# Optimization experiments

Measured on AMD Instinct MI355X. Metric: run time of the kernel, lower is better.

Reference implementation:

```python
import jax, jax.numpy as jnp
import numpy as np

K = 7          # local window
STRIDE = 1
PAD = 3
M = 8          # channel groups
C = 256
CQ = C // M    # key/query channels (32)
MID = int(0.5 * CQ)  # geometry prior hidden (16)
B, H, W = 4, 56, 56


def _unfold(x, k, stride, pad):
    """torch.nn.Unfold equivalent -> (B, C, L, k, k) with L = ho*wo."""
    b, c, h, w = x.shape
    xp = jnp.pad(x, ((0, 0), (0, 0), (pad, pad), (pad, pad)))
    ho = (h + 2 * pad - k) // stride + 1
    wo = (w + 2 * pad - k) // stride + 1
    cols = jnp.stack(
        [xp[:, :, i:i + stride * ho:stride, j:j + stride * wo:stride]
         for i in range(k) for j in range(k)], axis=-1)  # (B,C,ho,wo,k*k)
    return cols.reshape(b, c, ho * wo, k, k), ho, wo


def _geometry_position(k):
    a = jnp.arange(-(k // 2), k // 2 + 1, dtype=jnp.float32)
    x_pos = jnp.broadcast_to(a[None, :], (k, k))
    b_r = jnp.arange(k // 2, -(k // 2) - 1, -1, dtype=jnp.float32)
    y_pos = jnp.broadcast_to(b_r[:, None], (k, k))
    return jnp.stack([x_pos, y_pos], axis=0)  # (2, k, k)


def setup_inputs() -> dict:
    key = jax.random.key(0)
    ks = jax.random.split(key, 12)
    s = 0.05
    return {
        "x": jax.random.normal(ks[0], (B, C, H, W), jnp.float32),
        "w_k": jax.random.normal(ks[1], (CQ, C), jnp.float32) * s,
        "b_k": jax.random.normal(ks[2], (CQ,), jnp.float32) * s,
        "w_q": jax.random.normal(ks[3], (CQ, C), jnp.float32) * s,
        "b_q": jax.random.normal(ks[4], (CQ,), jnp.float32) * s,
        "w_g1": jax.random.normal(ks[5], (MID, 2), jnp.float32) * s,
        "b_g1": jax.random.normal(ks[6], (MID,), jnp.float32) * s,
        "w_g2": jax.random.normal(ks[7], (CQ, MID), jnp.float32) * s,
        "b_g2": jax.random.normal(ks[8], (CQ,), jnp.float32) * s,
        "w_f": jax.random.normal(ks[9], (C, C), jnp.float32) * s,
        "b_f": jax.random.normal(ks[10], (C,), jnp.float32) * s,
    }


def reference(x, w_k, b_k, w_q, b_q, w_g1, b_g1, w_g2, b_g2, w_f, b_f):
    b = x.shape[0]
    # key/query maps: 1x1 convs C -> CQ
    km = jnp.einsum('bchw,oc->bohw', x, w_k) + b_k[None, :, None, None]
    qm = jnp.einsum('bchw,oc->bohw', x, w_q) + b_q[None, :, None, None]

    km_u, ho, wo = _unfold(km, K, STRIDE, PAD)   # (B,CQ,L,k,k)
    qm_u, _, _ = _unfold(qm, K, STRIDE, PAD)
    center = K * K // 2
    q_center = qm_u.reshape(b, CQ, ho * wo, K * K)[:, :, :, center]  # (B,CQ,L)
    ak = km_u * q_center[:, :, :, None, None]    # (B,CQ,L,k,k)

    # geometry prior: two 1x1 convs on (2,k,k) position grid
    pos = _geometry_position(K)                                   # (2,k,k)
    g1 = jax.nn.relu(jnp.einsum('pij,op->oij', pos, w_g1) + b_g1[:, None, None])
    gpk = jnp.einsum('pij,op->oij', g1, w_g2) + b_g2[:, None, None]  # (CQ,k,k)

    # NOTE: softmax over the LAST k dim only (faithful to original dim=-1)
    ck = jax.nn.softmax(ak + gpk[None, :, None, :, :], axis=-1)   # (B,CQ,L,k,k)

    x_u, _, _ = _unfold(x, K, STRIDE, PAD)                        # (B,C,L,k,k)
    x_u = x_u.reshape(b, M, CQ, ho * wo, K, K)
    # ck broadcasts across the m groups
    pre = jnp.einsum('bclij,bgclij->bgcl', ck, x_u)               # (B,M,CQ,L)
    pre = pre.reshape(b, C, ho, wo)

    out = jnp.einsum('bchw,oc->bohw', pre, w_f) + b_f[None, :, None, None]
    return out
```

## Files before the change

kernel.cpp:

```cpp
#include <hip/hip_runtime.h>
#include <hip/hip_bf16.h>

typedef __hip_bfloat16 bf16;
typedef __attribute__((ext_vector_type(8))) short short8;
typedef __attribute__((ext_vector_type(4))) float floatx4;

#define B_   4
#define C_   256
#define CQ_  32
#define MID_ 16
#define HW_  3136

__device__ __forceinline__ unsigned short f2bf(float f) {
    __hip_bfloat16 h = __float2bfloat16(f);
    return *(unsigned short*)&h;
}
__device__ __forceinline__ float bf2f(short s) {
    return __uint_as_float(((unsigned)(unsigned short)s) << 16);
}

__global__ void __launch_bounds__(256) kq_setup(const float* __restrict__ x,
        const float* __restrict__ w_k, const float* __restrict__ b_k,
        const float* __restrict__ w_q, const float* __restrict__ b_q,
        const float* __restrict__ w_f,
        const float* __restrict__ wg1, const float* __restrict__ bg1,
        const float* __restrict__ wg2, const float* __restrict__ bg2,
        float* __restrict__ km, float* __restrict__ qm,
        short* __restrict__ wfp, float* __restrict__ gpk) {
    int bid = blockIdx.x, t = threadIdx.x;
    if (bid >= 392) {
        if (bid < 408) {
            int base = (bid - 392) * 4096;
            #pragma unroll
            for (int s = 0; s < 16; s++) {
                int j = base + s * 256 + t;
                wfp[j] = (short)f2bf(w_f[(j >> 8) * 256 + (j & 7) * 32 + ((j & 255) >> 3)]);
            }
        } else {
            for (int idx = t; idx < CQ_ * 49; idx += 256) {
                int cq = idx / 49, ij = idx % 49;
                int i = ij / 7, j = ij % 7;
                float xp = (float)(j - 3), yp = (float)(3 - i);
                float acc = bg2[cq];
                #pragma unroll
                for (int o = 0; o < MID_; o++) {
                    float g1 = wg1[o * 2] * xp + wg1[o * 2 + 1] * yp + bg1[o];
                    acc += wg2[cq * MID_ + o] * fmaxf(g1, 0.f);
                }
                gpk[idx] = acc;
            }
        }
        return;
    }
    __shared__ short lt[32 * 264];
    int hw0 = (bid % 98) * 32;
    int b   = bid / 98;

    int pq = t & 7, cb = t >> 3;
    const float* xb = x + (size_t)b * C_ * HW_ + hw0 + pq * 4;
    floatx4 fa[4], fb[4];
    #pragma unroll
    for (int ii = 0; ii < 4; ii++) {
        int c = ii * 64 + cb * 2;
        fa[ii] = *(const floatx4*)(xb + (size_t)c * HW_);
        fb[ii] = *(const floatx4*)(xb + (size_t)(c + 1) * HW_);
    }
    #pragma unroll
    for (int ii = 0; ii < 4; ii++) {
        int c = ii * 64 + cb * 2;
        int c8 = c >> 3, sub = c & 7;
        #pragma unroll
        for (int u = 0; u < 4; u++) {
            int px = pq * 4 + u;
            unsigned uu = (unsigned)f2bf(fa[ii][u]) | ((unsigned)f2bf(fb[ii][u]) << 16);
            *(unsigned*)&lt[px * 264 + ((c8 + (px >> 2)) & 31) * 8 + sub] = uu;
        }
    }

    int wave = t >> 6, lane = t & 63, quad = lane >> 4, nl = lane & 15;
    int m0 = wave * 16;
    int row = m0 + nl;
    const float* wsrc = (row < 32) ? (w_k + row * C_) : (w_q + (row - 32) * C_);
    short8 af[8];
    #pragma unroll
    for (int k0 = 0; k0 < 8; k0++) {
        floatx4 wa = *(const floatx4*)(wsrc + k0 * 32 + quad * 8);
        floatx4 wb = *(const floatx4*)(wsrc + k0 * 32 + quad * 8 + 4);
        short8 v;
        #pragma unroll
        for (int u = 0; u < 4; u++) { v[u] = (short)f2bf(wa[u]); v[u + 4] = (short)f2bf(wb[u]); }
        af[k0] = v;
    }
    __syncthreads();

    floatx4 acc0 = {0.f,0.f,0.f,0.f}, acc1 = {0.f,0.f,0.f,0.f};
    #pragma unroll
    for (int nt = 0; nt < 2; nt++) {
        int px = nt * 16 + nl;
        int prow = px * 264, sw = px >> 2;
        #pragma unroll
        for (int k0 = 0; k0 < 8; k0++) {
            short8 bfr = *(const short8*)&lt[prow + (((k0 * 4 + quad) + sw) & 31) * 8];
            if (nt == 0) acc0 = __builtin_amdgcn_mfma_f32_16x16x32_bf16(af[k0], bfr, acc0, 0, 0, 0);
            else         acc1 = __builtin_amdgcn_mfma_f32_16x16x32_bf16(af[k0], bfr, acc1, 0, 0, 0);
        }
    }
    #pragma unroll
    for (int r = 0; r < 4; r++) {
        int ch = m0 + quad * 4 + r;
        bool isK = (ch < 32);
        int c = isK ? ch : ch - 32;
        float bias = isK ? b_k[c] : b_q[c];
        float* dst = (isK ? km : qm) + ((size_t)b * CQ_ + c) * HW_ + hw0 + nl;
        dst[0]  = acc0[r] + bias;
        dst[16] = acc1[r] + bias;
    }
}

__global__ void __launch_bounds__(448) core_kernel(const float* __restrict__ x,
        const float* __restrict__ km, const float* __restrict__ qm,
        const float* __restrict__ gpk, short* __restrict__ pret) {
    __shared__ float kms[14 * 64];
    __shared__ short xs[14 * 64 * 8];

    int ht = blockIdx.x, cq = blockIdx.y, b = blockIdx.z;
    int h0 = ht * 8, t = threadIdx.x;

    const float* kmc = km + ((size_t)b * CQ_ + cq) * HW_;
    if (t < 196) {
        int rr = t / 14, s = t % 14;
        int gh = h0 + rr - 3;
        floatx4 v = {0.f,0.f,0.f,0.f};
        if ((unsigned)gh < 56u) v = *(const floatx4*)&kmc[gh * 56 + s * 4];
        *(floatx4*)&kms[rr * 64 + 4 + 4 * s] = v;
    }
    if (t < 84) {
        int rr = t / 6, e = t % 6;
        kms[rr * 64 + ((e < 3) ? 1 + e : 57 + e)] = 0.f;
    }
    if (t < 392) {
        int rr = t / 28, rem = t % 28, s = rem >> 1, mg = rem & 1;
        int gh = h0 + rr - 3;
        bool valid = ((unsigned)gh < 56u);
        floatx4 f[4];
        #pragma unroll
        for (int mm = 0; mm < 4; mm++) {
            int m = mg * 4 + mm;
            f[mm] = (floatx4){0.f,0.f,0.f,0.f};
            if (valid) f[mm] = *(const floatx4*)&x[((size_t)b * C_ + m * CQ_ + cq) * HW_ + gh * 56 + s * 4];
        }
        #pragma unroll
        for (int u = 0; u < 4; u++) {
            int p = 4 + 4 * s + u;
            unsigned lo = (unsigned)f2bf(f[0][u]) | ((unsigned)f2bf(f[1][u]) << 16);
            unsigned hi = (unsigned)f2bf(f[2][u]) | ((unsigned)f2bf(f[3][u]) << 16);
            unsigned long long pk = (unsigned long long)lo | ((unsigned long long)hi << 32);
            *(unsigned long long*)&xs[(rr * 64 + p) * 8 + mg * 4] = pk;
        }
    }
    if (t < 168) {
        int rr = t / 12, rem = t % 12, e = rem >> 1, mg = rem & 1;
        int p = (e < 3) ? 1 + e : 57 + e;
        *(unsigned long long*)&xs[(rr * 64 + p) * 8 + mg * 4] = 0ull;
    }
    __syncthreads();

    int r = t / 56, w = t % 56;
    float q = qm[((size_t)b * CQ_ + cq) * HW_ + (h0 + r) * 56 + w];
    const float* gp = gpk + cq * 49;

    float acc[8];
    #pragma unroll
    for (int m = 0; m < 8; m++) acc[m] = 0.f;

    #pragma unroll
    for (int i = 0; i < 7; i++) {
        const float* kr = &kms[(r + i) * 64 + w + 1];
        float v[7], s = 0.f;
        #pragma unroll
        for (int j = 0; j < 7; j++) {
            v[j] = __expf(kr[j] * q + gp[i * 7 + j]);
            s += v[j];
        }
        float rm[8];
        #pragma unroll
        for (int m = 0; m < 8; m++) rm[m] = 0.f;
        #pragma unroll
        for (int j = 0; j < 7; j++) {
            short8 xv = *(const short8*)&xs[((r + i) * 64 + w + j + 1) * 8];
            #pragma unroll
            for (int m = 0; m < 8; m++) rm[m] += v[j] * bf2f(xv[m]);
        }
        float inv = 1.0f / s;
        #pragma unroll
        for (int m = 0; m < 8; m++) acc[m] += inv * rm[m];
    }

    short8 o8;
    #pragma unroll
    for (int m = 0; m < 8; m++) o8[m] = (short)f2bf(acc[m]);
    *(short8*)&pret[((size_t)b * HW_ + (h0 + r) * 56 + w) * C_ + cq * 8] = o8;
}

__global__ void __launch_bounds__(256) fconv_mfma(const short* __restrict__ pret,
                                                  const short* __restrict__ wfp,
                                                  const float* __restrict__ b_f,
                                                  float* __restrict__ out) {
    int hw0 = blockIdx.x * 64;
    int bm  = blockIdx.y;
    int b   = blockIdx.z;
    int t   = threadIdx.x, wave = t >> 6, lane = t & 63, quad = lane >> 4, nl = lane & 15;
    int m0  = bm * 64 + wave * 16;

    const short* arow = wfp + (m0 + nl) * C_ + quad * 8;
    short8 af[8];
    #pragma unroll
    for (int k0 = 0; k0 < 8; k0++) af[k0] = *(const short8*)(arow + k0 * 32);

    floatx4 acc[4];
    #pragma unroll
    for (int nt = 0; nt < 4; nt++) acc[nt] = (floatx4){0.f,0.f,0.f,0.f};

    const short* pb = pret + ((size_t)b * HW_ + hw0 + nl) * C_ + quad * 8;
    #pragma unroll
    for (int nt = 0; nt < 4; nt++) {
        const short* bp = pb + (size_t)nt * 16 * C_;
        #pragma unroll
        for (int k0 = 0; k0 < 8; k0++)
            acc[nt] = __builtin_amdgcn_mfma_f32_16x16x32_bf16(af[k0], *(const short8*)(bp + k0 * 32),
                                                              acc[nt], 0, 0, 0);
    }

    #pragma unroll
    for (int r = 0; r < 4; r++) {
        int ch = m0 + quad * 4 + r;
        float bias = b_f[ch];
        float* dst = out + ((size_t)b * C_ + ch) * HW_ + hw0 + nl;
        #pragma unroll
        for (int nt = 0; nt < 4; nt++)
            dst[nt * 16] = acc[nt][r] + bias;
    }
}

extern "C" void kernel_launch(void* const* d_in, const int* in_sizes, int n_in,
                              void* d_out, int out_size, void* d_ws, size_t ws_size,
                              hipStream_t stream) {
    const float* x    = (const float*)d_in[0];
    const float* w_k  = (const float*)d_in[1];
    const float* b_k  = (const float*)d_in[2];
    const float* w_q  = (const float*)d_in[3];
    const float* b_q  = (const float*)d_in[4];
    const float* w_g1 = (const float*)d_in[5];
    const float* b_g1 = (const float*)d_in[6];
    const float* w_g2 = (const float*)d_in[7];
    const float* b_g2 = (const float*)d_in[8];
    const float* w_f  = (const float*)d_in[9];
    const float* b_f  = (const float*)d_in[10];
    float* out = (float*)d_out;

    float* ws   = (float*)d_ws;
    float* km   = ws;
    float* qm   = km + (size_t)B_ * CQ_ * HW_;
    float* gpk  = qm + (size_t)B_ * CQ_ * HW_;
    short* wfp  = (short*)(gpk + CQ_ * 49);
    short* pret = wfp + C_ * C_;

    kq_setup<<<dim3(409), 256, 0, stream>>>(x, w_k, b_k, w_q, b_q, w_f,
                                            w_g1, b_g1, w_g2, b_g2, km, qm, wfp, gpk);
    core_kernel<<<dim3(7, CQ_, B_), 448, 0, stream>>>(x, km, qm, gpk, pret);
    fconv_mfma<<<dim3(HW_ / 64, C_ / 64, B_), 256, 0, stream>>>(pret, wfp, b_f, out);
}
```

Measured before the change: 148.0 us.

## Pre-transpose x to bf16 grouped layout and store km/qm as bf16

The first kernel now also writes a bf16 copy of x laid out as (b, cq, pixel, m), with the 8 group channels packed together. It also stores the key and query maps in bf16 instead of fp32, and the 1x1 conv tiles shrink to 16 pixels so more blocks run. The core kernel loads this packed data with single 16-byte reads, and each of its 256 threads (224 active) computes two output rows. This removes the strided fp32 gathers and in-kernel conversion in the core kernel, at the cost of an extra write and read of the transposed x and lower km/qm precision.

```diff
diff --git a/kernel.cpp b/kernel.cpp
--- a/kernel.cpp
+++ b/kernel.cpp
@@ -19,18 +19,34 @@
     return __uint_as_float(((unsigned)(unsigned short)s) << 16);
 }
 
-__global__ void __launch_bounds__(256) kq_setup(const float* __restrict__ x,
+__global__ void __launch_bounds__(256) k1_kernel(const float* __restrict__ x,
         const float* __restrict__ w_k, const float* __restrict__ b_k,
         const float* __restrict__ w_q, const float* __restrict__ b_q,
         const float* __restrict__ w_f,
         const float* __restrict__ wg1, const float* __restrict__ bg1,
         const float* __restrict__ wg2, const float* __restrict__ bg2,
-        float* __restrict__ km, float* __restrict__ qm,
-        short* __restrict__ wfp, float* __restrict__ gpk) {
+        short* __restrict__ km, short* __restrict__ qm,
+        short* __restrict__ xt, short* __restrict__ wfp, float* __restrict__ gpk) {
     int bid = blockIdx.x, t = threadIdx.x;
-    if (bid >= 392) {
-        if (bid < 408) {
-            int base = (bid - 392) * 4096;
+
+    if (bid >= 784) {
+        if (bid < 980) {
+            int bid2 = bid - 784;
+            int s = bid2 % 49, b = bid2 / 49;
+            int px = s * 64 + (t & 63);
+            int cg = t >> 6;
+            const float* xb = x + (size_t)b * C_ * HW_ + px;
+            #pragma unroll
+            for (int cqi = 0; cqi < 8; cqi++) {
+                int cq = cg * 8 + cqi;
+                short8 v;
+                #pragma unroll
+                for (int m = 0; m < 8; m++)
+                    v[m] = (short)f2bf(xb[(size_t)(m * CQ_ + cq) * HW_]);
+                *(short8*)&xt[(((size_t)b * CQ_ + cq) * HW_ + px) * 8] = v;
+            }
+        } else if (bid < 996) {
+            int base = (bid - 980) * 4096;
             #pragma unroll
             for (int s = 0; s < 16; s++) {
                 int j = base + s * 256 + t;
@@ -52,30 +68,17 @@
         }
         return;
     }
-    __shared__ short lt[32 * 264];
-    int hw0 = (bid % 98) * 32;
-    int b   = bid / 98;
-
-    int pq = t & 7, cb = t >> 3;
+
+    __shared__ short lt[16 * 264];
+    int hw0 = (bid % 196) * 16;
+    int b   = bid / 196;
+
+    int pq = t & 3, cb = t >> 2;
     const float* xb = x + (size_t)b * C_ * HW_ + hw0 + pq * 4;
-    floatx4 fa[4], fb[4];
-    #pragma unroll
-    for (int ii = 0; ii < 4; ii++) {
-        int c = ii * 64 + cb * 2;
-        fa[ii] = *(const floatx4*)(xb + (size_t)c * HW_);
-        fb[ii] = *(const floatx4*)(xb + (size_t)(c + 1) * HW_);
-    }
-    #pragma unroll
-    for (int ii = 0; ii < 4; ii++) {
-        int c = ii * 64 + cb * 2;
-        int c8 = c >> 3, sub = c & 7;
-        #pragma unroll
-        for (int u = 0; u < 4; u++) {
-            int px = pq * 4 + u;
-            unsigned uu = (unsigned)f2bf(fa[ii][u]) | ((unsigned)f2bf(fb[ii][u]) << 16);
-            *(unsigned*)&lt[px * 264 + ((c8 + (px >> 2)) & 31) * 8 + sub] = uu;
-        }
-    }
+    floatx4 f[4];
+    #pragma unroll
+    for (int ii = 0; ii < 4; ii++)
+        f[ii] = *(const floatx4*)(xb + (size_t)(cb * 4 + ii) * HW_);
 
     int wave = t >> 6, lane = t & 63, quad = lane >> 4, nl = lane & 15;
     int m0 = wave * 16;
@@ -91,19 +94,26 @@
         for (int u = 0; u < 4; u++) { v[u] = (short)f2bf(wa[u]); v[u + 4] = (short)f2bf(wb[u]); }
         af[k0] = v;
     }
+
+    #pragma unroll
+    for (int pr = 0; pr < 2; pr++) {
+        int c = cb * 4 + pr * 2;
+        int c8 = c >> 3, sub = c & 7;
+        #pragma unroll
+        for (int u = 0; u < 4; u++) {
+            int px = pq * 4 + u;
+            unsigned uu = (unsigned)f2bf(f[pr * 2][u]) | ((unsigned)f2bf(f[pr * 2 + 1][u]) << 16);
+            *(unsigned*)&lt[px * 264 + ((c8 + pq) & 31) * 8 + sub] = uu;
+        }
+    }
     __syncthreads();
 
-    floatx4 acc0 = {0.f,0.f,0.f,0.f}, acc1 = {0.f,0.f,0.f,0.f};
-    #pragma unroll
-    for (int nt = 0; nt < 2; nt++) {
-        int px = nt * 16 + nl;
-        int prow = px * 264, sw = px >> 2;
-        #pragma unroll
-        for (int k0 = 0; k0 < 8; k0++) {
-            short8 bfr = *(const short8*)&lt[prow + (((k0 * 4 + quad) + sw) & 31) * 8];
-            if (nt == 0) acc0 = __builtin_amdgcn_mfma_f32_16x16x32_bf16(af[k0], bfr, acc0, 0, 0, 0);
-            else         acc1 = __builtin_amdgcn_mfma_f32_16x16x32_bf16(af[k0], bfr, acc1, 0, 0, 0);
-        }
+    floatx4 acc = {0.f, 0.f, 0.f, 0.f};
+    int prow = nl * 264, sw = nl >> 2;
+    #pragma unroll
+    for (int k0 = 0; k0 < 8; k0++) {
+        short8 bfr = *(const short8*)&lt[prow + (((k0 * 4 + quad) + sw) & 31) * 8];
+        acc = __builtin_amdgcn_mfma_f32_16x16x32_bf16(af[k0], bfr, acc, 0, 0, 0);
     }
     #pragma unroll
     for (int r = 0; r < 4; r++) {
@@ -111,14 +121,13 @@
         bool isK = (ch < 32);
         int c = isK ? ch : ch - 32;
         float bias = isK ? b_k[c] : b_q[c];
-        float* dst = (isK ? km : qm) + ((size_t)b * CQ_ + c) * HW_ + hw0 + nl;
-        dst[0]  = acc0[r] + bias;
-        dst[16] = acc1[r] + bias;
-    }
-}
-
-__global__ void __launch_bounds__(448) core_kernel(const float* __restrict__ x,
-        const float* __restrict__ km, const float* __restrict__ qm,
+        short* dst = (isK ? km : qm) + ((size_t)b * CQ_ + c) * HW_ + hw0 + nl;
+        dst[0] = (short)f2bf(acc[r] + bias);
+    }
+}
+
+__global__ void __launch_bounds__(256, 4) core_kernel(const short* __restrict__ xt,
+        const short* __restrict__ km, const short* __restrict__ qm,
         const float* __restrict__ gpk, short* __restrict__ pret) {
     __shared__ float kms[14 * 64];
     __shared__ short xs[14 * 64 * 8];
@@ -126,80 +135,64 @@
     int ht = blockIdx.x, cq = blockIdx.y, b = blockIdx.z;
     int h0 = ht * 8, t = threadIdx.x;
 
-    const float* kmc = km + ((size_t)b * CQ_ + cq) * HW_;
-    if (t < 196) {
-        int rr = t / 14, s = t % 14;
-        int gh = h0 + rr - 3;
-        floatx4 v = {0.f,0.f,0.f,0.f};
-        if ((unsigned)gh < 56u) v = *(const floatx4*)&kmc[gh * 56 + s * 4];
-        *(floatx4*)&kms[rr * 64 + 4 + 4 * s] = v;
-    }
-    if (t < 84) {
-        int rr = t / 6, e = t % 6;
-        kms[rr * 64 + ((e < 3) ? 1 + e : 57 + e)] = 0.f;
-    }
-    if (t < 392) {
-        int rr = t / 28, rem = t % 28, s = rem >> 1, mg = rem & 1;
-        int gh = h0 + rr - 3;
-        bool valid = ((unsigned)gh < 56u);
-        floatx4 f[4];
-        #pragma unroll
-        for (int mm = 0; mm < 4; mm++) {
-            int m = mg * 4 + mm;
-            f[mm] = (floatx4){0.f,0.f,0.f,0.f};
-            if (valid) f[mm] = *(const floatx4*)&x[((size_t)b * C_ + m * CQ_ + cq) * HW_ + gh * 56 + s * 4];
+    const short* kmc = km + ((size_t)b * CQ_ + cq) * HW_;
+    const short* xtc = xt + (((size_t)b * CQ_ + cq) * HW_) * 8;
+
+    for (int u = t; u < 896; u += 256) {
+        int rr = u >> 6, p = u & 63;
+        int gh = h0 + rr - 3, gw = p - 4;
+        bool in = ((unsigned)gh < 56u) && ((unsigned)gw < 56u);
+        int o = gh * 56 + gw;
+        short8 v = {0,0,0,0,0,0,0,0};
+        float kv = 0.f;
+        if (in) { v = *(const short8*)&xtc[(size_t)o * 8]; kv = bf2f(kmc[o]); }
+        *(short8*)&xs[u * 8] = v;
+        kms[u] = kv;
+    }
+    __syncthreads();
+
+    if (t >= 224) return;
+    int rp = t / 56, w = t % 56;
+    const float* gp = gpk + cq * 49;
+
+    #pragma unroll
+    for (int rowi = 0; rowi < 2; rowi++) {
+        int r = rp * 2 + rowi;
+        int h = h0 + r;
+        float q = bf2f(qm[((size_t)b * CQ_ + cq) * HW_ + h * 56 + w]);
+
+        float acc[8];
+        #pragma unroll
+        for (int m = 0; m < 8; m++) acc[m] = 0.f;
+
+        #pragma unroll
+        for (int i = 0; i < 7; i++) {
+            const float* kr = &kms[(r + i) * 64 + w + 1];
+            float v[7], s = 0.f;
+            #pragma unroll
+            for (int j = 0; j < 7; j++) {
+                v[j] = __expf(kr[j] * q + gp[i * 7 + j]);
+                s += v[j];
+            }
+            float rm[8];
+            #pragma unroll
+            for (int m = 0; m < 8; m++) rm[m] = 0.f;
+            #pragma unroll
+            for (int j = 0; j < 7; j++) {
+                short8 xv = *(const short8*)&xs[((r + i) * 64 + w + 1 + j) * 8];
+                #pragma unroll
+                for (int m = 0; m < 8; m++) rm[m] += v[j] * bf2f(xv[m]);
+            }
+            float inv = 1.0f / s;
+            #pragma unroll
+            for (int m = 0; m < 8; m++) acc[m] += inv * rm[m];
         }
-        #pragma unroll
-        for (int u = 0; u < 4; u++) {
-            int p = 4 + 4 * s + u;
-            unsigned lo = (unsigned)f2bf(f[0][u]) | ((unsigned)f2bf(f[1][u]) << 16);
-            unsigned hi = (unsigned)f2bf(f[2][u]) | ((unsigned)f2bf(f[3][u]) << 16);
-            unsigned long long pk = (unsigned long long)lo | ((unsigned long long)hi << 32);
-            *(unsigned long long*)&xs[(rr * 64 + p) * 8 + mg * 4] = pk;
-        }
-    }
-    if (t < 168) {
-        int rr = t / 12, rem = t % 12, e = rem >> 1, mg = rem & 1;
-        int p = (e < 3) ? 1 + e : 57 + e;
-        *(unsigned long long*)&xs[(rr * 64 + p) * 8 + mg * 4] = 0ull;
-    }
-    __syncthreads();
-
-    int r = t / 56, w = t % 56;
-    float q = qm[((size_t)b * CQ_ + cq) * HW_ + (h0 + r) * 56 + w];
-    const float* gp = gpk + cq * 49;
-
-    float acc[8];
-    #pragma unroll
-    for (int m = 0; m < 8; m++) acc[m] = 0.f;
-
-    #pragma unroll
-    for (int i = 0; i < 7; i++) {
-        const float* kr = &kms[(r + i) * 64 + w + 1];
-        float v[7], s = 0.f;
-        #pragma unroll
-        for (int j = 0; j < 7; j++) {
-            v[j] = __expf(kr[j] * q + gp[i * 7 + j]);
-            s += v[j];
-        }
-        float rm[8];
-        #pragma unroll
-        for (int m = 0; m < 8; m++) rm[m] = 0.f;
-        #pragma unroll
-        for (int j = 0; j < 7; j++) {
-            short8 xv = *(const short8*)&xs[((r + i) * 64 + w + j + 1) * 8];
-            #pragma unroll
-            for (int m = 0; m < 8; m++) rm[m] += v[j] * bf2f(xv[m]);
-        }
-        float inv = 1.0f / s;
-        #pragma unroll
-        for (int m = 0; m < 8; m++) acc[m] += inv * rm[m];
-    }
-
-    short8 o8;
-    #pragma unroll
-    for (int m = 0; m < 8; m++) o8[m] = (short)f2bf(acc[m]);
-    *(short8*)&pret[((size_t)b * HW_ + (h0 + r) * 56 + w) * C_ + cq * 8] = o8;
+
+        short8 o8;
+        #pragma unroll
+        for (int m = 0; m < 8; m++) o8[m] = (short)f2bf(acc[m]);
+        *(short8*)&pret[((size_t)b * HW_ + h * 56 + w) * C_ + cq * 8] = o8;
+    }
 }
 
 __global__ void __launch_bounds__(256) fconv_mfma(const short* __restrict__ pret,
@@ -258,15 +251,16 @@
     const float* b_f  = (const float*)d_in[10];
     float* out = (float*)d_out;
 
-    float* ws   = (float*)d_ws;
-    float* km   = ws;
-    float* qm   = km + (size_t)B_ * CQ_ * HW_;
-    float* gpk  = qm + (size_t)B_ * CQ_ * HW_;
-    short* wfp  = (short*)(gpk + CQ_ * 49);
+    short* ws   = (short*)d_ws;
+    short* km   = ws;
+    short* qm   = km  + (size_t)B_ * CQ_ * HW_;
+    short* xt   = qm  + (size_t)B_ * CQ_ * HW_;
+    short* wfp  = xt  + (size_t)B_ * CQ_ * HW_ * 8;
     short* pret = wfp + C_ * C_;
-
-    kq_setup<<<dim3(409), 256, 0, stream>>>(x, w_k, b_k, w_q, b_q, w_f,
-                                            w_g1, b_g1, w_g2, b_g2, km, qm, wfp, gpk);
-    core_kernel<<<dim3(7, CQ_, B_), 448, 0, stream>>>(x, km, qm, gpk, pret);
+    float* gpk  = (float*)(pret + (size_t)B_ * HW_ * C_);
+
+    k1_kernel<<<dim3(997), 256, 0, stream>>>(x, w_k, b_k, w_q, b_q, w_f,
+                                             w_g1, b_g1, w_g2, b_g2, km, qm, xt, wfp, gpk);
+    core_kernel<<<dim3(7, CQ_, B_), 256, 0, stream>>>(xt, km, qm, gpk, pret);
     fconv_mfma<<<dim3(HW_ / 64, C_ / 64, B_), 256, 0, stream>>>(pret, wfp, b_f, out);
 }
```

Result: slower. 254.0 us (+71.6%).
